# Kernel optimization log

Hardware: AMD Instinct MI355X
Metric: run time of the kernel (lower is better)

The kernel has to match this reference:

```python
import jax, jax.numpy as jnp
import numpy as np
from jax import lax

SEQ, B, I, H, OUT = 256, 64, 256, 1024, 1024


def setup_inputs() -> dict:
    key = jax.random.key(0)
    ks = jax.random.split(key, 9)
    s_i = 1.0 / np.sqrt(I)
    s_h = 1.0 / np.sqrt(H)
    s_f = 1.0 / np.sqrt(2 * H)
    # Gate order: i, f, o, c (stacked along last dim -> 4H). Biases of the
    # x-linear and h-linear are summed in the cell, so a single combined bias
    # per gate is mathematically identical.
    return {
        "x": jax.random.normal(ks[0], (SEQ, B, I), dtype=jnp.float32),
        "Wx_f": jax.random.uniform(ks[1], (I, 4 * H), jnp.float32, -s_i, s_i),
        "Wh_f": jax.random.uniform(ks[2], (H, 4 * H), jnp.float32, -s_h, s_h),
        "b_f": jax.random.uniform(ks[3], (4 * H,), jnp.float32, -s_h, s_h),
        "Wx_b": jax.random.uniform(ks[4], (I, 4 * H), jnp.float32, -s_i, s_i),
        "Wh_b": jax.random.uniform(ks[5], (H, 4 * H), jnp.float32, -s_h, s_h),
        "b_b": jax.random.uniform(ks[6], (4 * H,), jnp.float32, -s_h, s_h),
        "W_fc": jax.random.uniform(ks[7], (2 * H, OUT), jnp.float32, -s_f, s_f),
        "b_fc": jax.random.uniform(ks[8], (OUT,), jnp.float32, -s_f, s_f),
    }


def _lstm_dir(x, Wx, Wh, b, reverse):
    B_, H_ = x.shape[1], Wh.shape[0]
    # Precompute input projections for all timesteps in one big GEMM.
    xg = jnp.einsum("tbi,ig->tbg", x, Wx) + b  # [T, B, 4H]

    def step(carry, xg_t):
        c, h = carry
        g = xg_t + h @ Wh  # [B, 4H]
        i, f, o, cg = jnp.split(g, 4, axis=-1)
        new_c = jax.nn.sigmoid(f) * c + jax.nn.sigmoid(i) * jnp.tanh(cg)
        new_h = jax.nn.sigmoid(o) * jnp.tanh(new_c)
        return (new_c, new_h), new_h

    init = (jnp.zeros((B_, H_), x.dtype), jnp.zeros((B_, H_), x.dtype))
    (c_last, h_last), hs = lax.scan(step, init, xg, reverse=reverse)
    # lax.scan(reverse=True) returns hs aligned to the original time order,
    # matching outputs_backward.insert(0, ...) in the torch code.
    return hs, h_last, c_last


def reference(x, Wx_f, Wh_f, b_f, Wx_b, Wh_b, b_b, W_fc, b_fc):
    hs_f, hF, cF = _lstm_dir(x, Wx_f, Wh_f, b_f, reverse=False)
    hs_b, hB, cB = _lstm_dir(x, Wx_b, Wh_b, b_b, reverse=True)
    combined = jnp.concatenate([hs_f, hs_b], axis=-1)  # [T, B, 2H]
    outputs = jnp.einsum("tbh,ho->tbo", combined, W_fc) + b_fc
    return outputs, ((hF, hB), (cF, cB))
```

## Files before the change

kernel.cpp:

```cpp
#include <hip/hip_runtime.h>

using short8 = __attribute__((ext_vector_type(8))) short;
using f32x4  = __attribute__((ext_vector_type(4))) float;

typedef unsigned short u16;
typedef unsigned int   u32;
typedef unsigned long long u64;

#define T_SEQ 256
#define BATCH 64
#define INP   256
#define HID   1024
#define GDIM  4096
#define KC    1280
#define OUTD  1024

#define NSL   40
#define NBLK  256
#define DBLK  128
#define LDSB  (NSL * 2 * 64 * 8 * 2)

#define MFMA16(a,b,c) __builtin_amdgcn_mfma_f32_16x16x32_bf16(a,b,c,0,0,0)

__device__ __forceinline__ u16 f2bf(float f){
  union { float f; u32 u; } v; v.f = f;
  u32 r = v.u + 0x7fffu + ((v.u >> 16) & 1u);
  return (u16)(r >> 16);
}
__device__ __forceinline__ float sigm(float x){ return 1.f/(1.f+__expf(-x)); }
__device__ __forceinline__ float tanhf_(float x){ return 1.f - 2.f/(__expf(2.f*x)+1.f); }

__device__ __forceinline__ void ag_st_u32(u32* p, u32 v){
  __hip_atomic_store(p, v, __ATOMIC_RELAXED, __HIP_MEMORY_SCOPE_AGENT);
}
__device__ __forceinline__ u64 ag_ld_u64(const u64* p){
  return __hip_atomic_load(p, __ATOMIC_RELAXED, __HIP_MEMORY_SCOPE_AGENT);
}

template<int CTRL>
__device__ __forceinline__ float qperm(float v){
  union { float f; int i; } u; u.f = v;
  u.i = __builtin_amdgcn_mov_dpp(u.i, CTRL, 0xf, 0xf, true);
  return u.f;
}
#define QP_XOR1 177
#define QP_XOR2 78

__global__ void build_wc(const float* __restrict__ WhF, const float* __restrict__ WxF,
                         const float* __restrict__ WhB, const float* __restrict__ WxB,
                         u16* __restrict__ WcF, u16* __restrict__ WcB)
{
  const int z = blockIdx.z; const int dir = z >> 2, gate = z & 3;
  const float* Wh = dir ? WhB : WhF;
  const float* Wx = dir ? WxB : WxF;
  u16* Wc = dir ? WcB : WcF;
  const int k0 = blockIdx.x * 64, j0 = blockIdx.y * 64;
  __shared__ float tile[64][65];
  const int t = threadIdx.x;
  #pragma unroll
  for (int i = 0; i < 16; ++i) {
    int idx = i*256 + t; int kr = idx >> 6, jc = idx & 63;
    int k = k0 + kr;
    float v = (k < HID) ? Wh[(size_t)k*GDIM + gate*HID + j0 + jc]
                        : Wx[(size_t)(k-HID)*GDIM + gate*HID + j0 + jc];
    tile[kr][jc] = v;
  }
  __syncthreads();
  #pragma unroll
  for (int i = 0; i < 16; ++i) {
    int idx = i*256 + t; int jc = idx >> 6, kr = idx & 63;
    int j  = j0 + jc;
    int nb = j >> 3, jl = j & 7;
    int nt = jl & 1, rq = jl >> 1;
    int n  = nb*32 + nt*16 + rq*4 + gate;
    Wc[(size_t)n*KC + k0 + kr] = f2bf(tile[kr][jc]);
  }
}

__global__ void build_wfc(const float* __restrict__ Wfc, u16* __restrict__ WfcT)
{
  const int k0 = blockIdx.x * 64;
  const int n0 = blockIdx.y * 64;
  __shared__ float tile[64][65];
  const int t = threadIdx.x;
  #pragma unroll
  for (int i = 0; i < 16; ++i) {
    int idx = i*256 + t; int kr = idx >> 6, nc = idx & 63;
    tile[kr][nc] = Wfc[(size_t)(k0+kr)*OUTD + n0 + nc];
  }
  __syncthreads();
  #pragma unroll
  for (int i = 0; i < 16; ++i) {
    int idx = i*256 + t; int nc = idx >> 6, kr = idx & 63;
    WfcT[(size_t)(n0+nc)*2048 + k0 + kr] = f2bf(tile[kr][nc]);
  }
}

__global__ void conv_x(const float* __restrict__ x, u16* __restrict__ xb, int n)
{
  int i = (blockIdx.x * blockDim.x + threadIdx.x) * 4;
  if (i < n) {
    float4 v = *(const float4*)(x + i);
    u32 lo = (u32)f2bf(v.x) | ((u32)f2bf(v.y) << 16);
    u32 hi = (u32)f2bf(v.z) | ((u32)f2bf(v.w) << 16);
    *(uint2*)(xb + i) = make_uint2(lo, hi);
  }
}

__global__ __launch_bounds__(256, 1) void lstm_persist(
    const u16* __restrict__ WcF, const u16* __restrict__ WcB,
    const u16* __restrict__ xb,
    const float* __restrict__ bF, const float* __restrict__ bB,
    u32* __restrict__ hs2, float* __restrict__ out_tail, int* flags)
{
  extern __shared__ __align__(16) u16 Bs[];

  __builtin_amdgcn_fence(__ATOMIC_ACQUIRE, "agent");

  const int bid = blockIdx.x;
  const int dir = bid >> 7;
  const int nb  = bid & 127;
  const int n0  = nb * 32;
  const u16* __restrict__ Wc   = dir ? WcB : WcF;
  const float* __restrict__ bias = dir ? bB : bF;

  const int tid  = threadIdx.x;
  const int w    = tid >> 6, lane = tid & 63;
  const int r    = lane & 15, q = lane >> 4, rq = r >> 2;
  int* __restrict__ fl = flags + (dir * 4 + w) * DBLK;
  const u64* __restrict__ fl64 = (const u64*)fl;

  for (int c = tid; c < NSL * 128; c += 256) {
    int ks  = c >> 7;
    int rem = c & 127;
    int nt  = rem >> 6, l2 = rem & 63;
    *(short8*)&Bs[(size_t)c * 8] =
        *(const short8*)(Wc + (size_t)(n0 + nt*16 + (l2 & 15)) * KC + ks*32 + (l2 >> 4)*8);
  }
  #define BSF(ks, nt) (*(const short8*)&Bs[((size_t)(((ks)*2 + (nt))*64 + lane))*8])

  const int jbase = nb * 8;
  float bia[2][4];
  #pragma unroll
  for (int nt = 0; nt < 2; ++nt)
    #pragma unroll
    for (int g = 0; g < 4; ++g)
      bia[nt][g] = bias[g * HID + jbase + 2*rq + nt];

  float creg[2][4];
  #pragma unroll
  for (int nt = 0; nt < 2; ++nt)
    #pragma unroll
    for (int rg = 0; rg < 4; ++rg) creg[nt][rg] = 0.f;

  const int row_a = w * 16 + r;

  short8 xf[8];
  {
    const int tt0 = dir ? (T_SEQ - 1) : 0;
    const u16* axr = xb + ((size_t)tt0 * BATCH + row_a) * INP;
    #pragma unroll
    for (int kx = 0; kx < 8; ++kx) xf[kx] = *(const short8*)(axr + kx*32 + q*8);
  }
  __syncthreads();

  f32x4 accA[2], accB[2];
  accA[0] = (f32x4)(0.f); accA[1] = (f32x4)(0.f);
  accB[0] = (f32x4)(0.f); accB[1] = (f32x4)(0.f);
  #pragma unroll
  for (int kx = 0; kx < 8; ++kx) {
    accA[0] = MFMA16(xf[kx], BSF(32 + kx, 0), accA[0]);
    accA[1] = MFMA16(xf[kx], BSF(32 + kx, 1), accA[1]);
  }

  u64 pf = 0;

  for (int s = 0; s < T_SEQ; ++s) {
    const int tt = dir ? (T_SEQ - 1 - s) : s;

    if (s > 0) {
      while (true) {
        int ok = ((int)(pf & 0xffffffffu) >= s) && ((int)(pf >> 32) >= s);
        if (__all(ok)) break;
        pf = ag_ld_u64(fl64 + lane);
      }
      const int tp = dir ? tt + 1 : tt - 1;
      const u32* __restrict__ ar =
          hs2 + (((size_t)(tp * 2 + dir) * 128 + q) * 64 + row_a) * 4;
      short8 hA[32];
      #pragma unroll
      for (int i = 0; i < 32; ++i)
        hA[i] = *(const short8*)(ar + (size_t)i * 1024);
      #pragma unroll
      for (int i = 0; i < 16; ++i) {
        accA[0] = MFMA16(hA[i], BSF(i, 0), accA[0]);
        accA[1] = MFMA16(hA[i], BSF(i, 1), accA[1]);
        accB[0] = MFMA16(hA[16 + i], BSF(16 + i, 0), accB[0]);
        accB[1] = MFMA16(hA[16 + i], BSF(16 + i, 1), accB[1]);
      }
    }

    float hnv[2][4];
    #pragma unroll
    for (int nt = 0; nt < 2; ++nt) {
      #pragma unroll
      for (int rg = 0; rg < 4; ++rg) {
        float v  = accA[nt][rg] + accB[nt][rg];
        float x1 = qperm<QP_XOR1>(v);
        float x2 = qperm<QP_XOR2>(v);
        float x3 = qperm<QP_XOR2>(x1);
        float cn = sigm(x1 + bia[nt][1]) * creg[nt][rg] + sigm(v + bia[nt][0]) * tanhf_(x3 + bia[nt][3]);
        float hn = sigm(x2 + bia[nt][2]) * tanhf_(cn);
        creg[nt][rg] = cn; hnv[nt][rg] = hn;
      }
    }
    if ((r & 3) == 0) {
      u32* base = hs2 + (((size_t)(tt * 2 + dir) * 128 + nb) * 64 + w*16 + q*4) * 4 + rq;
      #pragma unroll
      for (int rg = 0; rg < 4; ++rg) {
        u32 packed = (u32)f2bf(hnv[0][rg]) | ((u32)f2bf(hnv[1][rg]) << 16);
        ag_st_u32(base + rg * 4, packed);
      }
    }

    if (s < T_SEQ - 1) {
      asm volatile("s_waitcnt vmcnt(0)" ::: "memory");
      if (lane == 0) ag_st_u32((u32*)(fl + nb), (u32)(s + 1));
      const int tn = dir ? tt - 1 : tt + 1;
      const u16* axr = xb + ((size_t)tn * BATCH + row_a) * INP;
      #pragma unroll
      for (int kx = 0; kx < 8; ++kx) xf[kx] = *(const short8*)(axr + kx*32 + q*8);
      pf = ag_ld_u64(fl64 + lane);
      accA[0] = (f32x4)(0.f); accA[1] = (f32x4)(0.f);
      accB[0] = (f32x4)(0.f); accB[1] = (f32x4)(0.f);
      #pragma unroll
      for (int kx = 0; kx < 8; ++kx) {
        accA[0] = MFMA16(xf[kx], BSF(32 + kx, 0), accA[0]);
        accA[1] = MFMA16(xf[kx], BSF(32 + kx, 1), accA[1]);
      }
    } else {
      if ((r & 3) == 0) {
        #pragma unroll
        for (int nt = 0; nt < 2; ++nt)
          #pragma unroll
          for (int rg = 0; rg < 4; ++rg) {
            int row = w * 16 + q * 4 + rg;
            int j   = jbase + 2*rq + nt;
            out_tail[dir * (BATCH * HID) + (size_t)row * HID + j] = hnv[nt][rg];
            out_tail[2 * (BATCH * HID) + dir * (BATCH * HID) + (size_t)row * HID + j] = creg[nt][rg];
          }
      }
    }
  }
  #undef BSF
}

__global__ __launch_bounds__(256) void fc_kernel(
    const u32* __restrict__ hs2, const u16* __restrict__ WfcT,
    const float* __restrict__ bfc, float* __restrict__ out)
{
  const int m0 = blockIdx.x * 128, n0 = blockIdx.y * 128;
  __shared__ __align__(16) u16 As[128 * 32];
  __shared__ __align__(16) u16 Bs[128 * 32];
  const int tid = threadIdx.x;
  const int w = tid >> 6, lane = tid & 63;
  const int r = lane & 15, q = lane >> 4;
  const int wy = w >> 1, wx = w & 1;

  f32x4 acc[4][4];
  #pragma unroll
  for (int a = 0; a < 4; ++a)
    #pragma unroll
    for (int b = 0; b < 4; ++b) acc[a][b] = (f32x4)(0.f);

  const int lr = tid >> 1, lk = (tid & 1) * 16;

  for (int k0 = 0; k0 < 2048; k0 += 32) {
    __syncthreads();
    {
      int m = m0 + lr; int t = m >> 6, row = m & 63;
      int k = k0 + lk; int d = k >> 10, kk = k & 1023; int nb2 = kk >> 3;
      const u32* p = hs2 + (((size_t)(t * 2 + d) * 128 + nb2) * 64 + row) * 4;
      *(short8*)&As[lr * 32 + lk]     = *(const short8*)p;
      *(short8*)&As[lr * 32 + lk + 8] = *(const short8*)(p + 256);
    }
    *(short8*)&Bs[lr * 32 + lk]     = *(const short8*)(WfcT + (size_t)(n0 + lr) * 2048 + k0 + lk);
    *(short8*)&Bs[lr * 32 + lk + 8] = *(const short8*)(WfcT + (size_t)(n0 + lr) * 2048 + k0 + lk + 8);
    __syncthreads();

    short8 af[4], bf[4];
    #pragma unroll
    for (int mt = 0; mt < 4; ++mt)
      af[mt] = *(const short8*)&As[(wy * 64 + mt * 16 + r) * 32 + q * 8];
    #pragma unroll
    for (int nt = 0; nt < 4; ++nt)
      bf[nt] = *(const short8*)&Bs[(wx * 64 + nt * 16 + r) * 32 + q * 8];
    #pragma unroll
    for (int mt = 0; mt < 4; ++mt)
      #pragma unroll
      for (int nt = 0; nt < 4; ++nt)
        acc[mt][nt] = __builtin_amdgcn_mfma_f32_16x16x32_bf16(af[mt], bf[nt], acc[mt][nt], 0, 0, 0);
  }

  #pragma unroll
  for (int mt = 0; mt < 4; ++mt)
    #pragma unroll
    for (int nt = 0; nt < 4; ++nt)
      #pragma unroll
      for (int reg = 0; reg < 4; ++reg) {
        int m = m0 + wy * 64 + mt * 16 + q * 4 + reg;
        int n = n0 + wx * 64 + nt * 16 + r;
        out[(size_t)m * OUTD + n] = acc[mt][nt][reg] + bfc[n];
      }
}

extern "C" void kernel_launch(void* const* d_in, const int* in_sizes, int n_in,
                              void* d_out, int out_size, void* d_ws, size_t ws_size,
                              hipStream_t stream)
{
  const float* x   = (const float*)d_in[0];
  const float* WxF = (const float*)d_in[1];
  const float* WhF = (const float*)d_in[2];
  const float* bF  = (const float*)d_in[3];
  const float* WxB = (const float*)d_in[4];
  const float* WhB = (const float*)d_in[5];
  const float* bB  = (const float*)d_in[6];
  const float* Wfc = (const float*)d_in[7];
  const float* bfc = (const float*)d_in[8];
  float* out = (float*)d_out;

  char* ws = (char*)d_ws;
  u16*  WcF   = (u16*)(ws + 0);
  u16*  WcB   = (u16*)(ws + 10485760);
  u16*  WfcT  = (u16*)(ws + 20971520);
  u16*  xb    = (u16*)(ws + 25165824);
  u32*  hs2   = (u32*)(ws + 34603008);
  int*  flags = (int*)(ws + 101711872);

  hipMemsetAsync(flags, 0, 4096, stream);

  hipFuncSetAttribute((const void*)lstm_persist,
                      hipFuncAttributeMaxDynamicSharedMemorySize, LDSB);

  build_wc <<<dim3(KC/64, HID/64, 8), 256, 0, stream>>>(WhF, WxF, WhB, WxB, WcF, WcB);
  build_wfc<<<dim3(2048/64, OUTD/64), 256, 0, stream>>>(Wfc, WfcT);
  conv_x   <<<(T_SEQ*BATCH*INP)/4/256, 256, 0, stream>>>(x, xb, T_SEQ*BATCH*INP);

  lstm_persist<<<NBLK, 256, LDSB, stream>>>(WcF, WcB, xb, bF, bB,
                                            hs2, out + 16777216, flags);

  fc_kernel<<<dim3(16384/128, OUTD/128), 256, 0, stream>>>(hs2, WfcT, bfc, out);
}
```

Before: 2.410 ms.

## Split persistent LSTM across 512 blocks with half-width column slices

Doubles the number of persistent recurrence blocks from 256 to 512, so each block owns 16 gate columns (4 hidden units) instead of 32, with half the LDS weight slice. Two blocks can now reside per CU, and per-step MFMA work per block halves. The price is twice as many flags to poll per step (two u64 loads per lane) and a cross-lane swizzle to pack bf16 pairs from adjacent blocks' halves into the shared hs2 layout. The weight packing in build_wc is changed to match the new column ordering.

```diff
diff --git a/kernel.cpp b/kernel.cpp
--- a/kernel.cpp
+++ b/kernel.cpp
@@ -16,9 +16,9 @@
 #define OUTD  1024
 
 #define NSL   40
-#define NBLK  256
-#define DBLK  128
-#define LDSB  (NSL * 2 * 64 * 8 * 2)
+#define NBLK  512
+#define DBLK  256
+#define LDSB  (NSL * 64 * 8 * 2)
 
 #define MFMA16(a,b,c) __builtin_amdgcn_mfma_f32_16x16x32_bf16(a,b,c,0,0,0)
 
@@ -70,9 +70,7 @@
   for (int i = 0; i < 16; ++i) {
     int idx = i*256 + t; int jc = idx >> 6, kr = idx & 63;
     int j  = j0 + jc;
-    int nb = j >> 3, jl = j & 7;
-    int nt = jl & 1, rq = jl >> 1;
-    int n  = nb*32 + nt*16 + rq*4 + gate;
+    int n  = (j >> 2)*16 + (j & 3)*4 + gate;
     Wc[(size_t)n*KC + k0 + kr] = f2bf(tile[kr][jc]);
   }
 }
@@ -107,7 +105,7 @@
   }
 }
 
-__global__ __launch_bounds__(256, 1) void lstm_persist(
+__global__ __launch_bounds__(256, 2) void lstm_persist(
     const u16* __restrict__ WcF, const u16* __restrict__ WcB,
     const u16* __restrict__ xb,
     const float* __restrict__ bF, const float* __restrict__ bB,
@@ -118,9 +116,11 @@
   __builtin_amdgcn_fence(__ATOMIC_ACQUIRE, "agent");
 
   const int bid = blockIdx.x;
-  const int dir = bid >> 7;
-  const int nb  = bid & 127;
-  const int n0  = nb * 32;
+  const int dir = bid >> 8;
+  const int nb  = bid & 255;
+  const int n0  = nb * 16;
+  const int pr  = nb >> 1;
+  const int sub = nb & 1;
   const u16* __restrict__ Wc   = dir ? WcB : WcF;
   const float* __restrict__ bias = dir ? bB : bF;
 
@@ -130,28 +130,19 @@
   int* __restrict__ fl = flags + (dir * 4 + w) * DBLK;
   const u64* __restrict__ fl64 = (const u64*)fl;
 
-  for (int c = tid; c < NSL * 128; c += 256) {
-    int ks  = c >> 7;
-    int rem = c & 127;
-    int nt  = rem >> 6, l2 = rem & 63;
+  for (int c = tid; c < NSL * 64; c += 256) {
+    int ks = c >> 6, l = c & 63;
     *(short8*)&Bs[(size_t)c * 8] =
-        *(const short8*)(Wc + (size_t)(n0 + nt*16 + (l2 & 15)) * KC + ks*32 + (l2 >> 4)*8);
-  }
-  #define BSF(ks, nt) (*(const short8*)&Bs[((size_t)(((ks)*2 + (nt))*64 + lane))*8])
-
-  const int jbase = nb * 8;
-  float bia[2][4];
-  #pragma unroll
-  for (int nt = 0; nt < 2; ++nt)
-    #pragma unroll
-    for (int g = 0; g < 4; ++g)
-      bia[nt][g] = bias[g * HID + jbase + 2*rq + nt];
-
-  float creg[2][4];
-  #pragma unroll
-  for (int nt = 0; nt < 2; ++nt)
-    #pragma unroll
-    for (int rg = 0; rg < 4; ++rg) creg[nt][rg] = 0.f;
+        *(const short8*)(Wc + (size_t)(n0 + (l & 15)) * KC + ks*32 + (l >> 4)*8);
+  }
+  #define BSF(ks) (*(const short8*)&Bs[((size_t)((ks)*64 + lane))*8])
+
+  const int jcol = nb * 4 + rq;
+  float bia[4];
+  #pragma unroll
+  for (int g = 0; g < 4; ++g) bia[g] = bias[g * HID + jcol];
+
+  float creg[4] = {0.f, 0.f, 0.f, 0.f};
 
   const int row_a = w * 16 + r;
 
@@ -164,25 +155,22 @@
   }
   __syncthreads();
 
-  f32x4 accA[2], accB[2];
-  accA[0] = (f32x4)(0.f); accA[1] = (f32x4)(0.f);
-  accB[0] = (f32x4)(0.f); accB[1] = (f32x4)(0.f);
-  #pragma unroll
-  for (int kx = 0; kx < 8; ++kx) {
-    accA[0] = MFMA16(xf[kx], BSF(32 + kx, 0), accA[0]);
-    accA[1] = MFMA16(xf[kx], BSF(32 + kx, 1), accA[1]);
-  }
-
-  u64 pf = 0;
+  f32x4 accA = (f32x4)(0.f), accB = (f32x4)(0.f);
+  #pragma unroll
+  for (int kx = 0; kx < 8; ++kx) accA = MFMA16(xf[kx], BSF(32 + kx), accA);
+
+  u64 pf0 = 0, pf1 = 0;
 
   for (int s = 0; s < T_SEQ; ++s) {
     const int tt = dir ? (T_SEQ - 1 - s) : s;
 
     if (s > 0) {
       while (true) {
-        int ok = ((int)(pf & 0xffffffffu) >= s) && ((int)(pf >> 32) >= s);
+        int ok = ((int)(pf0 & 0xffffffffu) >= s) && ((int)(pf0 >> 32) >= s) &&
+                 ((int)(pf1 & 0xffffffffu) >= s) && ((int)(pf1 >> 32) >= s);
         if (__all(ok)) break;
-        pf = ag_ld_u64(fl64 + lane);
+        pf0 = ag_ld_u64(fl64 + lane);
+        pf1 = ag_ld_u64(fl64 + 64 + lane);
       }
       const int tp = dir ? tt + 1 : tt - 1;
       const u32* __restrict__ ar =
@@ -193,33 +181,31 @@
         hA[i] = *(const short8*)(ar + (size_t)i * 1024);
       #pragma unroll
       for (int i = 0; i < 16; ++i) {
-        accA[0] = MFMA16(hA[i], BSF(i, 0), accA[0]);
-        accA[1] = MFMA16(hA[i], BSF(i, 1), accA[1]);
-        accB[0] = MFMA16(hA[16 + i], BSF(16 + i, 0), accB[0]);
-        accB[1] = MFMA16(hA[16 + i], BSF(16 + i, 1), accB[1]);
-      }
-    }
-
-    float hnv[2][4];
-    #pragma unroll
-    for (int nt = 0; nt < 2; ++nt) {
+        accA = MFMA16(hA[i],      BSF(i),      accA);
+        accB = MFMA16(hA[16 + i], BSF(16 + i), accB);
+      }
+    }
+
+    float hnv[4];
+    #pragma unroll
+    for (int rg = 0; rg < 4; ++rg) {
+      float v  = accA[rg] + accB[rg];
+      float x1 = qperm<QP_XOR1>(v);
+      float x2 = qperm<QP_XOR2>(v);
+      float x3 = qperm<QP_XOR2>(x1);
+      float cn = sigm(x1 + bia[1]) * creg[rg] + sigm(v + bia[0]) * tanhf_(x3 + bia[3]);
+      float hn = sigm(x2 + bia[2]) * tanhf_(cn);
+      creg[rg] = cn; hnv[rg] = hn;
+    }
+    {
+      u32* base = hs2 + (((size_t)(tt * 2 + dir) * 128 + pr) * 64 + w*16 + q*4) * 4
+                      + sub * 2 + (r >> 3);
       #pragma unroll
       for (int rg = 0; rg < 4; ++rg) {
-        float v  = accA[nt][rg] + accB[nt][rg];
-        float x1 = qperm<QP_XOR1>(v);
-        float x2 = qperm<QP_XOR2>(v);
-        float x3 = qperm<QP_XOR2>(x1);
-        float cn = sigm(x1 + bia[nt][1]) * creg[nt][rg] + sigm(v + bia[nt][0]) * tanhf_(x3 + bia[nt][3]);
-        float hn = sigm(x2 + bia[nt][2]) * tanhf_(cn);
-        creg[nt][rg] = cn; hnv[nt][rg] = hn;
-      }
-    }
-    if ((r & 3) == 0) {
-      u32* base = hs2 + (((size_t)(tt * 2 + dir) * 128 + nb) * 64 + w*16 + q*4) * 4 + rq;
-      #pragma unroll
-      for (int rg = 0; rg < 4; ++rg) {
-        u32 packed = (u32)f2bf(hnv[0][rg]) | ((u32)f2bf(hnv[1][rg]) << 16);
-        ag_st_u32(base + rg * 4, packed);
+        u32 v32 = (u32)f2bf(hnv[rg]);
+        u32 ot  = (u32)__builtin_amdgcn_ds_swizzle((int)v32, 0x101F);
+        if ((r & 7) == 0)
+          ag_st_u32(base + rg * 4, v32 | (ot << 16));
       }
     }
 
@@ -230,25 +216,19 @@
       const u16* axr = xb + ((size_t)tn * BATCH + row_a) * INP;
       #pragma unroll
       for (int kx = 0; kx < 8; ++kx) xf[kx] = *(const short8*)(axr + kx*32 + q*8);
-      pf = ag_ld_u64(fl64 + lane);
-      accA[0] = (f32x4)(0.f); accA[1] = (f32x4)(0.f);
-      accB[0] = (f32x4)(0.f); accB[1] = (f32x4)(0.f);
-      #pragma unroll
-      for (int kx = 0; kx < 8; ++kx) {
-        accA[0] = MFMA16(xf[kx], BSF(32 + kx, 0), accA[0]);
-        accA[1] = MFMA16(xf[kx], BSF(32 + kx, 1), accA[1]);
-      }
+      pf0 = ag_ld_u64(fl64 + lane);
+      pf1 = ag_ld_u64(fl64 + 64 + lane);
+      accA = (f32x4)(0.f); accB = (f32x4)(0.f);
+      #pragma unroll
+      for (int kx = 0; kx < 8; ++kx) accA = MFMA16(xf[kx], BSF(32 + kx), accA);
     } else {
       if ((r & 3) == 0) {
         #pragma unroll
-        for (int nt = 0; nt < 2; ++nt)
-          #pragma unroll
-          for (int rg = 0; rg < 4; ++rg) {
-            int row = w * 16 + q * 4 + rg;
-            int j   = jbase + 2*rq + nt;
-            out_tail[dir * (BATCH * HID) + (size_t)row * HID + j] = hnv[nt][rg];
-            out_tail[2 * (BATCH * HID) + dir * (BATCH * HID) + (size_t)row * HID + j] = creg[nt][rg];
-          }
+        for (int rg = 0; rg < 4; ++rg) {
+          int row = w * 16 + q * 4 + rg;
+          out_tail[dir * (BATCH * HID) + (size_t)row * HID + jcol] = hnv[rg];
+          out_tail[2 * (BATCH * HID) + dir * (BATCH * HID) + (size_t)row * HID + jcol] = creg[rg];
+        }
       }
     }
   }
@@ -279,8 +259,8 @@
     __syncthreads();
     {
       int m = m0 + lr; int t = m >> 6, row = m & 63;
-      int k = k0 + lk; int d = k >> 10, kk = k & 1023; int nb2 = kk >> 3;
-      const u32* p = hs2 + (((size_t)(t * 2 + d) * 128 + nb2) * 64 + row) * 4;
+      int k = k0 + lk; int d = k >> 10, kk = k & 1023; int p2 = kk >> 3;
+      const u32* p = hs2 + (((size_t)(t * 2 + d) * 128 + p2) * 64 + row) * 4;
       *(short8*)&As[lr * 32 + lk]     = *(const short8*)p;
       *(short8*)&As[lr * 32 + lk + 8] = *(const short8*)(p + 256);
     }
@@ -337,7 +317,7 @@
   u32*  hs2   = (u32*)(ws + 34603008);
   int*  flags = (int*)(ws + 101711872);
 
-  hipMemsetAsync(flags, 0, 4096, stream);
+  hipMemsetAsync(flags, 0, 8192, stream);
 
   hipFuncSetAttribute((const void*)lstm_persist,
                       hipFuncAttributeMaxDynamicSharedMemorySize, LDSB);
```

Measured after the change: 5.056 ms. 110% more time.

## Pipeline per-group flag waits with h loads and MFMAs in LSTM step

Applied to the files above, without the earlier changes.

Replaces the wait-for-all-producers spin loop with a per-group wait. A ballot over the flag lanes lets each group of four k-chunks be loaded as soon as its eight producer blocks have published, and the loads are interleaved with the MFMAs of earlier groups through a four-deep register rotation. The aim is to overlap the inter-block synchronisation latency and global loads with compute on the recurrent critical path. The cost is more control flow, repeated flag polling inside the step, and a changed accumulation order across the A and B accumulators.

```diff
diff --git a/kernel.cpp b/kernel.cpp
--- a/kernel.cpp
+++ b/kernel.cpp
@@ -175,29 +175,49 @@
 
   u64 pf = 0;
 
+  #define WAITG(g) \
+    while (((bal >> (8*(g))) & 0xffull) != 0xffull) { \
+      pf  = ag_ld_u64(fl64 + lane); \
+      okv = ((int)(pf & 0xffffffffu) >= s) && ((int)(pf >> 32) >= s); \
+      bal = __ballot(okv); \
+    }
+  #define LOADG(B, g) \
+    B[0] = *(const short8*)(ar + (size_t)((g)*4 + 0) * 1024); \
+    B[1] = *(const short8*)(ar + (size_t)((g)*4 + 1) * 1024); \
+    B[2] = *(const short8*)(ar + (size_t)((g)*4 + 2) * 1024); \
+    B[3] = *(const short8*)(ar + (size_t)((g)*4 + 3) * 1024);
+  #define MFMAG(B, g) \
+    accA[0] = MFMA16(B[0], BSF((g)*4 + 0, 0), accA[0]); \
+    accA[1] = MFMA16(B[0], BSF((g)*4 + 0, 1), accA[1]); \
+    accB[0] = MFMA16(B[1], BSF((g)*4 + 1, 0), accB[0]); \
+    accB[1] = MFMA16(B[1], BSF((g)*4 + 1, 1), accB[1]); \
+    accA[0] = MFMA16(B[2], BSF((g)*4 + 2, 0), accA[0]); \
+    accA[1] = MFMA16(B[2], BSF((g)*4 + 2, 1), accA[1]); \
+    accB[0] = MFMA16(B[3], BSF((g)*4 + 3, 0), accB[0]); \
+    accB[1] = MFMA16(B[3], BSF((g)*4 + 3, 1), accB[1]);
+
   for (int s = 0; s < T_SEQ; ++s) {
     const int tt = dir ? (T_SEQ - 1 - s) : s;
 
     if (s > 0) {
-      while (true) {
-        int ok = ((int)(pf & 0xffffffffu) >= s) && ((int)(pf >> 32) >= s);
-        if (__all(ok)) break;
-        pf = ag_ld_u64(fl64 + lane);
-      }
+      int okv = ((int)(pf & 0xffffffffu) >= s) && ((int)(pf >> 32) >= s);
+      u64 bal = __ballot(okv);
       const int tp = dir ? tt + 1 : tt - 1;
       const u32* __restrict__ ar =
           hs2 + (((size_t)(tp * 2 + dir) * 128 + q) * 64 + row_a) * 4;
-      short8 hA[32];
-      #pragma unroll
-      for (int i = 0; i < 32; ++i)
-        hA[i] = *(const short8*)(ar + (size_t)i * 1024);
-      #pragma unroll
-      for (int i = 0; i < 16; ++i) {
-        accA[0] = MFMA16(hA[i], BSF(i, 0), accA[0]);
-        accA[1] = MFMA16(hA[i], BSF(i, 1), accA[1]);
-        accB[0] = MFMA16(hA[16 + i], BSF(16 + i, 0), accB[0]);
-        accB[1] = MFMA16(hA[16 + i], BSF(16 + i, 1), accB[1]);
-      }
+      short8 B0[4], B1[4], B2[4], B3[4];
+      WAITG(0) LOADG(B0, 0)
+      WAITG(1) LOADG(B1, 1)
+      WAITG(2) LOADG(B2, 2)
+      WAITG(3) LOADG(B3, 3)
+      MFMAG(B0, 0) WAITG(4) LOADG(B0, 4)
+      MFMAG(B1, 1) WAITG(5) LOADG(B1, 5)
+      MFMAG(B2, 2) WAITG(6) LOADG(B2, 6)
+      MFMAG(B3, 3) WAITG(7) LOADG(B3, 7)
+      MFMAG(B0, 4)
+      MFMAG(B1, 5)
+      MFMAG(B2, 6)
+      MFMAG(B3, 7)
     }
 
     float hnv[2][4];
@@ -253,6 +273,9 @@
     }
   }
   #undef BSF
+  #undef WAITG
+  #undef LOADG
+  #undef MFMAG
 }
 
 __global__ __launch_bounds__(256) void fc_kernel(
```

Result: slower. 2.652 ms (+10.0%).
